# Performance work log

Measured on AMD Instinct MI355X. Metric: run time of the kernel, lower is better.

## Reference

```python
import jax, jax.numpy as jnp
import numpy as np

N, D_DIM, K, R = 100000, 256, 4, 16
E_RAND = 1600000
ETA, LAM, C = 0.5, 0.1, 0.5


def setup_inputs() -> dict:
    key = jax.random.key(0)
    k1, k2, k3, k4 = jax.random.split(key, 4)
    Z = jax.random.normal(k1, (N, D_DIM), jnp.float32)
    U = jax.random.normal(k2, (K, D_DIM, R), jnp.float32) / np.float32(np.sqrt(D_DIM))
    Dmat = jax.random.normal(k3, (D_DIM, D_DIM), jnp.float32) / np.float32(np.sqrt(D_DIM))
    head_w = jnp.ones((K,), jnp.float32) / K
    rnd = jax.random.randint(k4, (2, E_RAND), 0, N)
    loops = jnp.stack([jnp.arange(N), jnp.arange(N)])  # self-loops: every node has an in-edge
    edge_index = jnp.concatenate([rnd, loops], axis=1)  # [2, E]
    return {"Z": Z, "U": U, "Dmat": Dmat, "head_w": head_w, "edge_index": edge_index}


def reference(Z, U, Dmat, head_w, edge_index):
    src, dst = edge_index[0], edge_index[1]
    scale = np.float32(np.sqrt(R))

    # Project into all K subspaces at once: [K, n, r]
    ZU = jnp.einsum('nd,kdr->knr', Z, U)
    zs = ZU[:, src, :]                      # [K, E, r] gather at src
    zd = ZU[:, dst, :]                      # [K, E, r] gather at dst
    logits = (zs * zd).sum(-1) / scale      # [K, E]

    seg_max = jax.vmap(lambda l: jax.ops.segment_max(l, dst, num_segments=N))(logits)
    exp_l = jnp.exp(logits - seg_max[:, dst])
    seg_sum = jax.vmap(lambda e: jax.ops.segment_sum(e, dst, num_segments=N))(exp_l)
    alpha = exp_l / (seg_sum[:, dst] + 1e-16)  # [K, E]

    weighted = alpha[..., None] * zs           # [K, E, r]
    agg = jax.vmap(lambda w_: jax.ops.segment_sum(w_, dst, num_segments=N))(weighted)  # [K, n, r]

    w = jax.nn.softmax(head_w)
    ssa = jnp.einsum('k,knr,kdr->nd', w, agg, U)  # sum_k w_k * (agg_k @ U_k^T)

    Z_half = (1.0 - C) * Z + C * ssa

    # ISTA step (matches torch code exactly):
    DZ = Z_half @ Dmat.T
    residual = Z_half - DZ @ Dmat
    grad_step = Z_half + ETA * (residual @ Dmat)
    return jax.nn.relu(grad_step - ETA * LAM)
```

## Files before the change

### kernel.cpp

```cpp
#include <hip/hip_runtime.h>
#include <stdint.h>


typedef unsigned short u16;
typedef unsigned int u32;
typedef __attribute__((ext_vector_type(8))) short bf16x8;
typedef __attribute__((ext_vector_type(4))) float f32x4;

#define PB 256

__device__ __forceinline__ u16 f2bf(float f) {
    u32 u = __float_as_uint(f);
    u32 r = u + 0x7fffu + ((u >> 16) & 1u);
    return (u16)(r >> 16);
}

__global__ void k_prep1(const float* __restrict__ D, float* __restrict__ G) {
    int i = blockIdx.x, j = threadIdx.x;
    float acc = 0.f;
    for (int d = 0; d < 256; ++d)
        acc += D[d * 256 + i] * D[d * 256 + j];
    G[i * 256 + j] = acc;
}

__global__ void k_prep2(const float* __restrict__ D, const float* __restrict__ G,
                        float* __restrict__ A) {
    int t = blockIdx.x, j = threadIdx.x;
    float acc = 0.f;
    for (int u = 0; u < 256; ++u)
        acc += G[t * 256 + u] * D[u * 256 + j];
    A[t * 256 + j] = 0.5f * (D[t * 256 + j] - acc) + (t == j ? 1.f : 0.f);
}

__global__ void k_prep3(const float* __restrict__ A, u16* __restrict__ Bt) {
    int c = blockIdx.x, k = threadIdx.x;
    Bt[c * 320 + k] = f2bf(0.5f * A[k * 256 + c]);
}

__global__ void k_prep4(const float* __restrict__ U, const float* __restrict__ A,
                        u16* __restrict__ Bt) {
    int j = blockIdx.x, c = threadIdx.x;
    int k = j >> 4, r = j & 15;
    float acc = 0.f;
    for (int d = 0; d < 256; ++d)
        acc += U[k * 4096 + d * 16 + r] * A[d * 256 + c];
    Bt[c * 320 + 256 + j] = f2bf(0.5f * acc);
}

__global__ __launch_bounds__(256) void k_cnt1(const int* __restrict__ ei,
                                              int* __restrict__ cnt2, int E, int nbuck) {
    __shared__ int h[512];
    int t = threadIdx.x, b = blockIdx.x;
    for (int i = t; i < nbuck; i += 256) h[i] = 0;
    __syncthreads();
    int per = (E + PB - 1) / PB;
    int lo = b * per;
    int hi = lo + per; if (hi > E) hi = E;
    for (int e = lo + t; e < hi; e += 256)
        atomicAdd(&h[ei[E + e] >> 8], 1);
    __syncthreads();
    for (int i = t; i < nbuck; i += 256)
        cnt2[b * nbuck + i] = h[i];
}

__global__ __launch_bounds__(256) void k_cscan1(const int* __restrict__ cnt2,
                                                int* __restrict__ pre2,
                                                int* __restrict__ tot, int nbuck) {
    __shared__ int s[256];
    int t = threadIdx.x, b = blockIdx.x;
    int v = cnt2[t * nbuck + b];
    s[t] = v;
    __syncthreads();
    for (int o = 1; o < 256; o <<= 1) {
        int x = (t >= o) ? s[t - o] : 0;
        __syncthreads();
        s[t] += x;
        __syncthreads();
    }
    pre2[t * nbuck + b] = s[t] - v;
    if (t == 255) tot[b] = s[255];
}

__global__ __launch_bounds__(512) void k_cscan2(const int* __restrict__ tot,
                                                int* __restrict__ bbase, int nbuck) {
    __shared__ int s[512];
    int t = threadIdx.x;
    int v = (t < nbuck) ? tot[t] : 0;
    s[t] = v;
    __syncthreads();
    for (int o = 1; o < 512; o <<= 1) {
        int x = (t >= o) ? s[t - o] : 0;
        __syncthreads();
        s[t] += x;
        __syncthreads();
    }
    if (t < nbuck) bbase[t] = s[t] - v;
}

__global__ __launch_bounds__(256) void k_place(const int* __restrict__ ei,
                                               const int* __restrict__ pre2,
                                               const int* __restrict__ bbase,
                                               int* __restrict__ part, int E, int nbuck) {
    __shared__ int baseS[512];
    __shared__ int cur[512];
    int t = threadIdx.x, b = blockIdx.x;
    for (int i = t; i < nbuck; i += 256) {
        baseS[i] = bbase[i] + pre2[b * nbuck + i];
        cur[i] = 0;
    }
    __syncthreads();
    int per = (E + PB - 1) / PB;
    int lo = b * per;
    int hi = lo + per; if (hi > E) hi = E;
    for (int e = lo + t; e < hi; e += 256) {
        int s = ei[e];
        int d = ei[E + e];
        int bk = d >> 8;
        int r = atomicAdd(&cur[bk], 1);
        part[baseS[bk] + r] = (s << 8) | (d & 255);
    }
}

__global__ __launch_bounds__(256) void k_bucket(const int* __restrict__ part,
                                                const int* __restrict__ tot,
                                                const int* __restrict__ bbase,
                                                int* __restrict__ off,
                                                int* __restrict__ cnt,
                                                int* __restrict__ esrc, int n) {
    __shared__ int ncnt[256], excl[256], cur[256], sc[256];
    int t = threadIdx.x, b = blockIdx.x;
    ncnt[t] = 0;
    cur[t] = 0;
    __syncthreads();
    int base = bbase[b], m = tot[b];
    for (int i = t; i < m; i += 256)
        atomicAdd(&ncnt[part[base + i] & 255], 1);
    __syncthreads();
    int v = ncnt[t];
    sc[t] = v;
    __syncthreads();
    for (int o = 1; o < 256; o <<= 1) {
        int x = (t >= o) ? sc[t - o] : 0;
        __syncthreads();
        sc[t] += x;
        __syncthreads();
    }
    excl[t] = sc[t] - v;
    int node = b * 256 + t;
    if (node < n) {
        off[node] = base + excl[t];
        cnt[node] = v;
    }
    __syncthreads();
    for (int i = t; i < m; i += 256) {
        int pk = part[base + i];
        int j = pk & 255;
        int r = atomicAdd(&cur[j], 1);
        esrc[base + excl[j] + r] = pk >> 8;
    }
}

__global__ __launch_bounds__(256) void k_zu(const float* __restrict__ Z,
                                            const float* __restrict__ U,
                                            float* __restrict__ ZU,
                                            u16* __restrict__ Zb, int n) {
    __shared__ float Us[64 * 68];
    __shared__ float Zs[64 * 65];
    const int t = threadIdx.x;
    const int nb = blockIdx.x * 64;
    const int nc = t >> 2;
    const int c0 = (t & 3) * 16;
    const int nl_ld = t >> 2;
    const int dd_ld = (t & 3) * 16;
    const int dd_u = t >> 2;
    const int k_u = t & 3;
    float acc[16];
#pragma unroll
    for (int i = 0; i < 16; ++i) acc[i] = 0.f;

    for (int ch = 0; ch < 4; ++ch) {
        __syncthreads();
        {
            int gn = nb + nl_ld;
            int gcl = gn < n ? gn : n - 1;
            const float4* zp = reinterpret_cast<const float4*>(
                Z + (size_t)gcl * 256 + ch * 64 + dd_ld);
            float4 z0 = zp[0], z1 = zp[1], z2 = zp[2], z3 = zp[3];
            float msk = gn < n ? 1.f : 0.f;
            float zf[16] = {z0.x, z0.y, z0.z, z0.w, z1.x, z1.y, z1.z, z1.w,
                            z2.x, z2.y, z2.z, z2.w, z3.x, z3.y, z3.z, z3.w};
#pragma unroll
            for (int i = 0; i < 16; ++i)
                Zs[nl_ld * 65 + dd_ld + i] = zf[i] * msk;
            if (gn < n) {
                uint4 pk;
                pk.x = (u32)f2bf(zf[0]) | ((u32)f2bf(zf[1]) << 16);
                pk.y = (u32)f2bf(zf[2]) | ((u32)f2bf(zf[3]) << 16);
                pk.z = (u32)f2bf(zf[4]) | ((u32)f2bf(zf[5]) << 16);
                pk.w = (u32)f2bf(zf[6]) | ((u32)f2bf(zf[7]) << 16);
                uint4 pk2;
                pk2.x = (u32)f2bf(zf[8])  | ((u32)f2bf(zf[9]) << 16);
                pk2.y = (u32)f2bf(zf[10]) | ((u32)f2bf(zf[11]) << 16);
                pk2.z = (u32)f2bf(zf[12]) | ((u32)f2bf(zf[13]) << 16);
                pk2.w = (u32)f2bf(zf[14]) | ((u32)f2bf(zf[15]) << 16);
                uint4* zb = reinterpret_cast<uint4*>(
                    Zb + (size_t)gn * 256 + ch * 64 + dd_ld);
                zb[0] = pk;
                zb[1] = pk2;
            }
        }
        {
            const float4* up = reinterpret_cast<const float4*>(
                U + k_u * 4096 + (ch * 64 + dd_u) * 16);
            float4* us = reinterpret_cast<float4*>(&Us[dd_u * 68 + k_u * 16]);
            us[0] = up[0]; us[1] = up[1]; us[2] = up[2]; us[3] = up[3];
        }
        __syncthreads();
        for (int dd = 0; dd < 64; ++dd) {
            float z = Zs[nc * 65 + dd];
            const float4* uq = reinterpret_cast<const float4*>(&Us[dd * 68 + c0]);
            float4 a = uq[0], b = uq[1], c = uq[2], d4 = uq[3];
            acc[0] += z * a.x;  acc[1] += z * a.y;  acc[2] += z * a.z;  acc[3] += z * a.w;
            acc[4] += z * b.x;  acc[5] += z * b.y;  acc[6] += z * b.z;  acc[7] += z * b.w;
            acc[8] += z * c.x;  acc[9] += z * c.y;  acc[10] += z * c.z; acc[11] += z * c.w;
            acc[12] += z * d4.x; acc[13] += z * d4.y; acc[14] += z * d4.z; acc[15] += z * d4.w;
        }
    }
    int gn = nb + nc;
    if (gn < n) {
        float4* o = reinterpret_cast<float4*>(ZU + (size_t)gn * 64 + c0);
        o[0] = make_float4(acc[0], acc[1], acc[2], acc[3]);
        o[1] = make_float4(acc[4], acc[5], acc[6], acc[7]);
        o[2] = make_float4(acc[8], acc[9], acc[10], acc[11]);
        o[3] = make_float4(acc[12], acc[13], acc[14], acc[15]);
    }
}

__global__ __launch_bounds__(256) void k_agg(const float* __restrict__ ZU,
                                             const int* __restrict__ esrc,
                                             const int* __restrict__ off,
                                             const int* __restrict__ cnt,
                                             const float* __restrict__ hwp,
                                             u16* __restrict__ Vb, int n) {
    int node = blockIdx.x * 4 + (threadIdx.x >> 6);
    int lane = threadIdx.x & 63;
    if (node >= n) return;
    const int q = lane & 15;
    const int g = lane >> 4;
    float4 zd4 = *reinterpret_cast<const float4*>(&ZU[(size_t)node * 64 + q * 4]);
    int base = off[node];
    int deg = cnt[node];

    float ax = 0.f, ay = 0.f, az = 0.f, aw = 0.f, ssum = 0.f;
    for (int c0 = 0; c0 < deg; c0 += 4) {
        int e = c0 + g;
        bool valid = e < deg;
        int s = valid ? esrc[base + e] : 0;
        float4 zs4 = *reinterpret_cast<const float4*>(&ZU[(size_t)s * 64 + q * 4]);
        float p = zs4.x * zd4.x + zs4.y * zd4.y + zs4.z * zd4.z + zs4.w * zd4.w;
        p += __shfl_xor(p, 1);
        p += __shfl_xor(p, 2);
        float ew = valid ? __expf(p * 0.25f) : 0.f;
        ax += ew * zs4.x; ay += ew * zs4.y;
        az += ew * zs4.z; aw += ew * zs4.w;
        ssum += ew;
    }
    ax += __shfl_xor(ax, 16); ax += __shfl_xor(ax, 32);
    ay += __shfl_xor(ay, 16); ay += __shfl_xor(ay, 32);
    az += __shfl_xor(az, 16); az += __shfl_xor(az, 32);
    aw += __shfl_xor(aw, 16); aw += __shfl_xor(aw, 32);
    ssum += __shfl_xor(ssum, 16); ssum += __shfl_xor(ssum, 32);

    if (g == 0) {
        float h0 = hwp[0], h1 = hwp[1], h2 = hwp[2], h3 = hwp[3];
        float mx = fmaxf(fmaxf(h0, h1), fmaxf(h2, h3));
        float e0 = __expf(h0 - mx), e1 = __expf(h1 - mx),
              e2 = __expf(h2 - mx), e3 = __expf(h3 - mx);
        float es = e0 + e1 + e2 + e3;
        int hd = q >> 2;
        float wk = (hd == 0 ? e0 : hd == 1 ? e1 : hd == 2 ? e2 : e3) / es;
        float inv = wk / ssum;
        uint2 pk;
        pk.x = (u32)f2bf(ax * inv) | ((u32)f2bf(ay * inv) << 16);
        pk.y = (u32)f2bf(az * inv) | ((u32)f2bf(aw * inv) << 16);
        *reinterpret_cast<uint2*>(&Vb[(size_t)node * 64 + q * 4]) = pk;
    }
}

__global__ __launch_bounds__(256) void k_out(const u16* __restrict__ Zb,
                                             const u16* __restrict__ Vb,
                                             const u16* __restrict__ Bt,
                                             float* __restrict__ out, int n) {
    const int t = threadIdx.x;
    const int w = t >> 6;
    const int lane = t & 63;
    const int m16 = lane & 15;
    const int quad = lane >> 4;
    const int nb = blockIdx.x * 64;

    f32x4 acc[4][4];
#pragma unroll
    for (int mt = 0; mt < 4; ++mt)
#pragma unroll
        for (int nt = 0; nt < 4; ++nt)
            acc[mt][nt] = (f32x4){0.f, 0.f, 0.f, 0.f};

    int rowc[4];
#pragma unroll
    for (int mt = 0; mt < 4; ++mt) {
        int r = nb + mt * 16 + m16;
        rowc[mt] = r < n ? r : n - 1;
    }
    const u16* bbase4[4];
#pragma unroll
    for (int nt = 0; nt < 4; ++nt)
        bbase4[nt] = Bt + (size_t)(w * 64 + nt * 16 + m16) * 320 + quad * 8;

    for (int ks = 0; ks < 8; ++ks) {
        bf16x8 a[4], b[4];
#pragma unroll
        for (int mt = 0; mt < 4; ++mt)
            a[mt] = *reinterpret_cast<const bf16x8*>(
                Zb + (size_t)rowc[mt] * 256 + ks * 32 + quad * 8);
#pragma unroll
        for (int nt = 0; nt < 4; ++nt)
            b[nt] = *reinterpret_cast<const bf16x8*>(bbase4[nt] + ks * 32);
#pragma unroll
        for (int mt = 0; mt < 4; ++mt)
#pragma unroll
            for (int nt = 0; nt < 4; ++nt)
                acc[mt][nt] = __builtin_amdgcn_mfma_f32_16x16x32_bf16(
                    a[mt], b[nt], acc[mt][nt], 0, 0, 0);
    }
#pragma unroll
    for (int ks = 8; ks < 10; ++ks) {
        bf16x8 a[4], b[4];
#pragma unroll
        for (int mt = 0; mt < 4; ++mt)
            a[mt] = *reinterpret_cast<const bf16x8*>(
                Vb + (size_t)rowc[mt] * 64 + (ks - 8) * 32 + quad * 8);
#pragma unroll
        for (int nt = 0; nt < 4; ++nt)
            b[nt] = *reinterpret_cast<const bf16x8*>(bbase4[nt] + ks * 32);
#pragma unroll
        for (int mt = 0; mt < 4; ++mt)
#pragma unroll
            for (int nt = 0; nt < 4; ++nt)
                acc[mt][nt] = __builtin_amdgcn_mfma_f32_16x16x32_bf16(
                    a[mt], b[nt], acc[mt][nt], 0, 0, 0);
    }

#pragma unroll
    for (int mt = 0; mt < 4; ++mt) {
#pragma unroll
        for (int r = 0; r < 4; ++r) {
            int row = nb + mt * 16 + quad * 4 + r;
            if (row < n) {
#pragma unroll
                for (int nt = 0; nt < 4; ++nt) {
                    int col = w * 64 + nt * 16 + m16;
                    out[(size_t)row * 256 + col] =
                        fmaxf(acc[mt][nt][r] - 0.05f, 0.f);
                }
            }
        }
    }
}

extern "C" void kernel_launch(void* const* d_in, const int* in_sizes, int n_in,
                              void* d_out, int out_size, void* d_ws, size_t ws_size,
                              hipStream_t stream) {
    const float* Z  = (const float*)d_in[0];
    const float* U  = (const float*)d_in[1];
    const float* Dm = (const float*)d_in[2];
    const float* hw = (const float*)d_in[3];
    const int*   ei = (const int*)d_in[4];
    const int n = in_sizes[0] / 256;
    const int E = in_sizes[4] / 2;
    float* out = (float*)d_out;
    const int nbuck = (n + 255) >> 8;

    char* wp = (char*)d_ws;
    float* ZUb  = (float*)wp;
    u16* Zb     = (u16*)(wp + (size_t)n * 256);
    int* part   = (int*)Zb;
    int* cnt2   = part + E;
    int* pre2   = cnt2 + PB * nbuck;
    u16* Vb     = Zb + (size_t)n * 256;
    float* G    = (float*)(Vb + (size_t)n * 64);
    float* A    = G + 65536;
    u16* Bt     = (u16*)(A + 65536);
    int* esrc   = (int*)(Bt + 256 * 320);
    int* off    = esrc + E;
    int* cnt    = off + n;
    int* tot    = cnt + n;
    int* bbase  = tot + nbuck;

    k_prep1<<<256, 256, 0, stream>>>(Dm, G);
    k_prep2<<<256, 256, 0, stream>>>(Dm, G, A);
    k_prep3<<<256, 256, 0, stream>>>(A, Bt);
    k_prep4<<<64, 256, 0, stream>>>(U, A, Bt);

    k_cnt1<<<PB, 256, 0, stream>>>(ei, cnt2, E, nbuck);
    k_cscan1<<<nbuck, 256, 0, stream>>>(cnt2, pre2, tot, nbuck);
    k_cscan2<<<1, 512, 0, stream>>>(tot, bbase, nbuck);
    k_place<<<PB, 256, 0, stream>>>(ei, pre2, bbase, part, E, nbuck);
    k_bucket<<<nbuck, 256, 0, stream>>>(part, tot, bbase, off, cnt, esrc, n);

    k_zu<<<(n + 63) / 64, 256, 0, stream>>>(Z, U, ZUb, Zb, n);
    k_agg<<<(n + 3) / 4, 256, 0, stream>>>(ZUb, esrc, off, cnt, hw, Vb, n);
    k_out<<<(n + 63) / 64, 256, 0, stream>>>(Zb, Vb, Bt, out, n);
}
```

Measured before the change: 477.3 us.

## Compute Z·U projection with bf16 MFMA after a separate Z cast kernel

Replaces the fp32 LDS-tiled Z·U projection with a separate bf16 cast kernel followed by an MFMA 16x16x32 bf16 matmul that reads the cast Z and a pre-transposed bf16 copy of U. The aim is to move the projection off scalar FMA onto matrix cores. In exchange it adds an extra kernel pass that writes and then rereads Zb, and it lowers ZU precision to bf16 inputs, which affects the attention logits. A new prep kernel builds the transposed U in the workspace.

```diff
diff --git a/kernel.cpp b/kernel.cpp
--- a/kernel.cpp
+++ b/kernel.cpp
@@ -45,6 +45,11 @@
     for (int d = 0; d < 256; ++d)
         acc += U[k * 4096 + d * 16 + r] * A[d * 256 + c];
     Bt[c * 320 + 256 + j] = f2bf(0.5f * acc);
+}
+
+__global__ void k_prep5(const float* __restrict__ U, u16* __restrict__ U2t) {
+    int j = blockIdx.x, d = threadIdx.x;
+    U2t[j * 256 + d] = f2bf(U[(j >> 4) * 4096 + d * 16 + (j & 15)]);
 }
 
 __global__ __launch_bounds__(256) void k_cnt1(const int* __restrict__ ei,
@@ -160,79 +165,55 @@
     }
 }
 
-__global__ __launch_bounds__(256) void k_zu(const float* __restrict__ Z,
-                                            const float* __restrict__ U,
-                                            float* __restrict__ ZU,
-                                            u16* __restrict__ Zb, int n) {
-    __shared__ float Us[64 * 68];
-    __shared__ float Zs[64 * 65];
+__global__ __launch_bounds__(256) void k_cast(const float* __restrict__ Z,
+                                              u16* __restrict__ Zb, int total8) {
+    int i = blockIdx.x * 256 + threadIdx.x;
+    if (i >= total8) return;
+    const float4* zp = reinterpret_cast<const float4*>(Z + (size_t)i * 8);
+    float4 a = zp[0], b = zp[1];
+    uint4 pk;
+    pk.x = (u32)f2bf(a.x) | ((u32)f2bf(a.y) << 16);
+    pk.y = (u32)f2bf(a.z) | ((u32)f2bf(a.w) << 16);
+    pk.z = (u32)f2bf(b.x) | ((u32)f2bf(b.y) << 16);
+    pk.w = (u32)f2bf(b.z) | ((u32)f2bf(b.w) << 16);
+    *reinterpret_cast<uint4*>(Zb + (size_t)i * 8) = pk;
+}
+
+__global__ __launch_bounds__(256) void k_zumm(const u16* __restrict__ Zb,
+                                              const u16* __restrict__ U2t,
+                                              float* __restrict__ ZU, int n) {
     const int t = threadIdx.x;
-    const int nb = blockIdx.x * 64;
-    const int nc = t >> 2;
-    const int c0 = (t & 3) * 16;
-    const int nl_ld = t >> 2;
-    const int dd_ld = (t & 3) * 16;
-    const int dd_u = t >> 2;
-    const int k_u = t & 3;
-    float acc[16];
-#pragma unroll
-    for (int i = 0; i < 16; ++i) acc[i] = 0.f;
-
-    for (int ch = 0; ch < 4; ++ch) {
-        __syncthreads();
-        {
-            int gn = nb + nl_ld;
-            int gcl = gn < n ? gn : n - 1;
-            const float4* zp = reinterpret_cast<const float4*>(
-                Z + (size_t)gcl * 256 + ch * 64 + dd_ld);
-            float4 z0 = zp[0], z1 = zp[1], z2 = zp[2], z3 = zp[3];
-            float msk = gn < n ? 1.f : 0.f;
-            float zf[16] = {z0.x, z0.y, z0.z, z0.w, z1.x, z1.y, z1.z, z1.w,
-                            z2.x, z2.y, z2.z, z2.w, z3.x, z3.y, z3.z, z3.w};
-#pragma unroll
-            for (int i = 0; i < 16; ++i)
-                Zs[nl_ld * 65 + dd_ld + i] = zf[i] * msk;
-            if (gn < n) {
-                uint4 pk;
-                pk.x = (u32)f2bf(zf[0]) | ((u32)f2bf(zf[1]) << 16);
-                pk.y = (u32)f2bf(zf[2]) | ((u32)f2bf(zf[3]) << 16);
-                pk.z = (u32)f2bf(zf[4]) | ((u32)f2bf(zf[5]) << 16);
-                pk.w = (u32)f2bf(zf[6]) | ((u32)f2bf(zf[7]) << 16);
-                uint4 pk2;
-                pk2.x = (u32)f2bf(zf[8])  | ((u32)f2bf(zf[9]) << 16);
-                pk2.y = (u32)f2bf(zf[10]) | ((u32)f2bf(zf[11]) << 16);
-                pk2.z = (u32)f2bf(zf[12]) | ((u32)f2bf(zf[13]) << 16);
-                pk2.w = (u32)f2bf(zf[14]) | ((u32)f2bf(zf[15]) << 16);
-                uint4* zb = reinterpret_cast<uint4*>(
-                    Zb + (size_t)gn * 256 + ch * 64 + dd_ld);
-                zb[0] = pk;
-                zb[1] = pk2;
-            }
+    const int w = t >> 6;
+    const int lane = t & 63;
+    const int m16 = lane & 15;
+    const int quad = lane >> 4;
+    const int nb = blockIdx.x * 64 + w * 16;
+
+    int row = nb + m16;
+    int rowc = row < n ? row : n - 1;
+
+    f32x4 acc[4];
+#pragma unroll
+    for (int nt = 0; nt < 4; ++nt) acc[nt] = (f32x4){0.f, 0.f, 0.f, 0.f};
+
+    for (int ks = 0; ks < 8; ++ks) {
+        bf16x8 a = *reinterpret_cast<const bf16x8*>(
+            Zb + (size_t)rowc * 256 + ks * 32 + quad * 8);
+#pragma unroll
+        for (int nt = 0; nt < 4; ++nt) {
+            bf16x8 b = *reinterpret_cast<const bf16x8*>(
+                U2t + (size_t)(nt * 16 + m16) * 256 + ks * 32 + quad * 8);
+            acc[nt] = __builtin_amdgcn_mfma_f32_16x16x32_bf16(a, b, acc[nt], 0, 0, 0);
         }
-        {
-            const float4* up = reinterpret_cast<const float4*>(
-                U + k_u * 4096 + (ch * 64 + dd_u) * 16);
-            float4* us = reinterpret_cast<float4*>(&Us[dd_u * 68 + k_u * 16]);
-            us[0] = up[0]; us[1] = up[1]; us[2] = up[2]; us[3] = up[3];
+    }
+#pragma unroll
+    for (int r = 0; r < 4; ++r) {
+        int node = nb + quad * 4 + r;
+        if (node < n) {
+#pragma unroll
+            for (int nt = 0; nt < 4; ++nt)
+                ZU[(size_t)node * 64 + nt * 16 + m16] = acc[nt][r];
         }
-        __syncthreads();
-        for (int dd = 0; dd < 64; ++dd) {
-            float z = Zs[nc * 65 + dd];
-            const float4* uq = reinterpret_cast<const float4*>(&Us[dd * 68 + c0]);
-            float4 a = uq[0], b = uq[1], c = uq[2], d4 = uq[3];
-            acc[0] += z * a.x;  acc[1] += z * a.y;  acc[2] += z * a.z;  acc[3] += z * a.w;
-            acc[4] += z * b.x;  acc[5] += z * b.y;  acc[6] += z * b.z;  acc[7] += z * b.w;
-            acc[8] += z * c.x;  acc[9] += z * c.y;  acc[10] += z * c.z; acc[11] += z * c.w;
-            acc[12] += z * d4.x; acc[13] += z * d4.y; acc[14] += z * d4.z; acc[15] += z * d4.w;
-        }
-    }
-    int gn = nb + nc;
-    if (gn < n) {
-        float4* o = reinterpret_cast<float4*>(ZU + (size_t)gn * 64 + c0);
-        o[0] = make_float4(acc[0], acc[1], acc[2], acc[3]);
-        o[1] = make_float4(acc[4], acc[5], acc[6], acc[7]);
-        o[2] = make_float4(acc[8], acc[9], acc[10], acc[11]);
-        o[3] = make_float4(acc[12], acc[13], acc[14], acc[15]);
     }
 }
 
@@ -390,7 +371,8 @@
     float* G    = (float*)(Vb + (size_t)n * 64);
     float* A    = G + 65536;
     u16* Bt     = (u16*)(A + 65536);
-    int* esrc   = (int*)(Bt + 256 * 320);
+    u16* U2t    = Bt + 256 * 320;
+    int* esrc   = (int*)(U2t + 64 * 256);
     int* off    = esrc + E;
     int* cnt    = off + n;
     int* tot    = cnt + n;
@@ -400,6 +382,7 @@
     k_prep2<<<256, 256, 0, stream>>>(Dm, G, A);
     k_prep3<<<256, 256, 0, stream>>>(A, Bt);
     k_prep4<<<64, 256, 0, stream>>>(U, A, Bt);
+    k_prep5<<<64, 256, 0, stream>>>(U, U2t);
 
     k_cnt1<<<PB, 256, 0, stream>>>(ei, cnt2, E, nbuck);
     k_cscan1<<<nbuck, 256, 0, stream>>>(cnt2, pre2, tot, nbuck);
@@ -407,7 +390,8 @@
     k_place<<<PB, 256, 0, stream>>>(ei, pre2, bbase, part, E, nbuck);
     k_bucket<<<nbuck, 256, 0, stream>>>(part, tot, bbase, off, cnt, esrc, n);
 
-    k_zu<<<(n + 63) / 64, 256, 0, stream>>>(Z, U, ZUb, Zb, n);
+    k_cast<<<(n * 256 / 8 + 255) / 256, 256, 0, stream>>>(Z, Zb, n * 32);
+    k_zumm<<<(n + 63) / 64, 256, 0, stream>>>(Zb, U2t, ZUb, n);
     k_agg<<<(n + 3) / 4, 256, 0, stream>>>(ZUb, esrc, off, cnt, hw, Vb, n);
     k_out<<<(n + 63) / 64, 256, 0, stream>>>(Zb, Vb, Bt, out, n);
 }
```

After: 474.3 us. No clear change (-0.6%).
